# Kernel tuning notes

Hardware: AMD Instinct MI355X
Metric: run time of the kernel (lower is better)

The kernel has to match this reference:

```python
import jax, jax.numpy as jnp
import numpy as np

C = 64
C8 = C // 8
N, H, W = 4, 512, 512


def conv1x1(x, w, b):
    # x: [N,C,H,W], w: [O,C], b: [O]
    return jnp.einsum('nchw,oc->nohw', x, w) + b[None, :, None, None]


def time_attention(x, qw, qb, kw, kb, vw, vb, gamma):
    # attention over the H axis; feature dim is (C//8)*W
    q = conv1x1(x, qw, qb)                     # [N,C8,H,W]
    k = conv1x1(x, kw, kb)                     # [N,C8,H,W]
    v = conv1x1(x, vw, vb)                     # [N,C,H,W]
    energy = jnp.einsum('nchw,ncgw->nhg', q, k)   # [N,H,H]
    attn = jax.nn.softmax(energy, axis=-1)
    out = jnp.einsum('ncgw,nhg->nchw', v, attn)   # [N,C,H,W]
    return gamma * out + x


def freq_attention(x, qw, qb, kw, kb, vw, vb, gamma):
    # attention over the W axis; feature dim is (C//8)*H
    q = conv1x1(x, qw, qb)
    k = conv1x1(x, kw, kb)
    v = conv1x1(x, vw, vb)
    energy = jnp.einsum('nchw,nchv->nwv', q, k)   # [N,W,W]
    attn = jax.nn.softmax(energy, axis=-1)
    out = jnp.einsum('nchv,nwv->nchw', v, attn)
    return gamma * out + x


def setup_inputs() -> dict:
    key = jax.random.key(0)
    ks = jax.random.split(key, 8)
    s = 0.05
    return {
        'x': jax.random.normal(ks[0], (N, C, H, W), dtype=jnp.float32),
        'tq_w': jax.random.normal(ks[1], (C8, C), dtype=jnp.float32) * s,
        'tq_b': jnp.zeros((C8,), jnp.float32),
        'tk_w': jax.random.normal(ks[2], (C8, C), dtype=jnp.float32) * s,
        'tk_b': jnp.zeros((C8,), jnp.float32),
        'tv_w': jax.random.normal(ks[3], (C, C), dtype=jnp.float32) * s,
        'tv_b': jnp.zeros((C,), jnp.float32),
        't_gamma': jnp.ones((1,), jnp.float32) * 0.5,
        'fq_w': jax.random.normal(ks[4], (C8, C), dtype=jnp.float32) * s,
        'fq_b': jnp.zeros((C8,), jnp.float32),
        'fk_w': jax.random.normal(ks[5], (C8, C), dtype=jnp.float32) * s,
        'fk_b': jnp.zeros((C8,), jnp.float32),
        'fv_w': jax.random.normal(ks[6], (C, C), dtype=jnp.float32) * s,
        'fv_b': jnp.zeros((C,), jnp.float32),
        'f_gamma': jnp.ones((1,), jnp.float32) * 0.5,
    }


def reference(x, tq_w, tq_b, tk_w, tk_b, tv_w, tv_b, t_gamma,
              fq_w, fq_b, fk_w, fk_b, fv_w, fv_b, f_gamma):
    t = time_attention(x, tq_w, tq_b, tk_w, tk_b, tv_w, tv_b, t_gamma)
    f = freq_attention(x, fq_w, fq_b, fk_w, fk_b, fv_w, fv_b, f_gamma)
    return x + t + f
```

## Files before the change

### kernel.cpp

```cpp
#include <hip/hip_runtime.h>
#include <stdint.h>

#define HW 262144
#define LDIM 512

typedef __bf16 bf16x8 __attribute__((ext_vector_type(8)));
typedef float f32x4 __attribute__((ext_vector_type(4)));
typedef short s16x8 __attribute__((ext_vector_type(8)));
typedef short s16x4 __attribute__((ext_vector_type(4)));

__device__ __forceinline__ unsigned short f2bf(float f) {
  union { float f; unsigned u; } v; v.f = f;
  unsigned r = v.u + 0x7fffu + ((v.u >> 16) & 1u);
  return (unsigned short)(r >> 16);
}

__device__ __forceinline__ s16x8 pack_bf8(float4 a, float4 b) {
  s16x8 r;
  r[0] = (short)f2bf(a.x); r[1] = (short)f2bf(a.y);
  r[2] = (short)f2bf(a.z); r[3] = (short)f2bf(a.w);
  r[4] = (short)f2bf(b.x); r[5] = (short)f2bf(b.y);
  r[6] = (short)f2bf(b.z); r[7] = (short)f2bf(b.w);
  return r;
}

__device__ __forceinline__ f32x4 mfma16(bf16x8 a, bf16x8 b, f32x4 c) {
  return __builtin_amdgcn_mfma_f32_16x16x32_bf16(a, b, c, 0, 0, 0);
}

__global__ __launch_bounds__(256) void cast_k(const float* __restrict__ x,
                                              short* __restrict__ xb,
                                              short* __restrict__ xt) {
  __shared__ short L[64][72];
  int z = blockIdx.z;
  int h0 = blockIdx.y * 64, w0 = blockIdx.x * 64;
  int tid = threadIdx.x;
  size_t base = (size_t)z * HW;
  int hl = tid >> 4;
  int wl = (tid & 15) * 4;
#pragma unroll
  for (int it = 0; it < 4; ++it) {
    int h = h0 + hl + it * 16;
    float4 v = *(const float4*)(x + base + (size_t)h * 512 + w0 + wl);
    s16x4 b;
    b[0] = (short)f2bf(v.x); b[1] = (short)f2bf(v.y);
    b[2] = (short)f2bf(v.z); b[3] = (short)f2bf(v.w);
    *(s16x4*)(xb + base + (size_t)h * 512 + w0 + wl) = b;
    L[wl + 0][hl + it * 16] = b[0];
    L[wl + 1][hl + it * 16] = b[1];
    L[wl + 2][hl + it * 16] = b[2];
    L[wl + 3][hl + it * 16] = b[3];
  }
  __syncthreads();
#pragma unroll
  for (int it = 0; it < 4; ++it) {
    int w = hl + it * 16;
    s16x4 v = *(const s16x4*)(&L[w][wl]);
    *(s16x4*)(xt + base + (size_t)(w0 + w) * 512 + h0 + wl) = v;
  }
}

template<int MODE>
__device__ __forceinline__ void stage_tile(short* __restrict__ dst,
                                           const void* __restrict__ base,
                                           size_t eoff, int ld, int kk, int mn0,
                                           int tid) {
  if constexpr (MODE == 0) {
    int r = tid >> 1, off = (tid & 1) * 16;
    const short* s = (const short*)base + eoff + (size_t)(mn0 + r) * ld + kk + off;
    s16x8 v0 = *(const s16x8*)s;
    s16x8 v1 = *(const s16x8*)(s + 8);
    *(s16x8*)(dst + r * 40 + off) = v0;
    *(s16x8*)(dst + r * 40 + off + 8) = v1;
  } else {
    int mp = (tid & 63) * 2, k0 = (tid >> 6) * 8;
    const short* s = (const short*)base + eoff + (size_t)(kk + k0) * ld + mn0 + mp;
    s16x8 c0, c1;
#pragma unroll
    for (int j = 0; j < 8; ++j) {
      unsigned v = *(const unsigned*)(s + (size_t)j * ld);
      c0[j] = (short)(v & 0xffffu);
      c1[j] = (short)(v >> 16);
    }
    *(s16x8*)(dst + mp * 40 + k0) = c0;
    *(s16x8*)(dst + (mp + 1) * 40 + k0) = c1;
  }
}

template<int AM, int BM, bool OBF>
__global__ __launch_bounds__(256, 2) void gemm_k(
    const void* __restrict__ A0, long az, int zshA, int lda,
    const void* __restrict__ B0, long bz, int zshB, int ldb,
    void* __restrict__ C0, long cz) {
  __shared__ __align__(16) short As[128 * 40];
  __shared__ __align__(16) short Bs[128 * 40];
  int tid = threadIdx.x;
  int z = blockIdx.z;
  int m0g = blockIdx.y * 128, n0g = blockIdx.x * 128;
  size_t aoffz = (size_t)(z >> zshA) * (size_t)az;
  size_t boffz = (size_t)(z >> zshB) * (size_t)bz;
  int lane = tid & 63, wv = tid >> 6;
  int wm = (wv >> 1) * 64, wn = (wv & 1) * 64;
  int fr = lane & 15, q = lane >> 4;

  f32x4 acc[4][4];
#pragma unroll
  for (int mi = 0; mi < 4; ++mi)
#pragma unroll
    for (int ni = 0; ni < 4; ++ni) acc[mi][ni] = (f32x4){0.f, 0.f, 0.f, 0.f};

  for (int kidx = 0; kidx < 16; ++kidx) {
    int kk = kidx * 32;
    stage_tile<AM>(As, A0, aoffz, lda, kk, m0g, tid);
    stage_tile<BM>(Bs, B0, boffz, ldb, kk, n0g, tid);
    __syncthreads();
    bf16x8 af[4], bg[4];
#pragma unroll
    for (int mi = 0; mi < 4; ++mi)
      af[mi] = *(const bf16x8*)(As + (wm + mi * 16 + fr) * 40 + q * 8);
#pragma unroll
    for (int ni = 0; ni < 4; ++ni)
      bg[ni] = *(const bf16x8*)(Bs + (wn + ni * 16 + fr) * 40 + q * 8);
#pragma unroll
    for (int mi = 0; mi < 4; ++mi)
#pragma unroll
      for (int ni = 0; ni < 4; ++ni)
        acc[mi][ni] = mfma16(af[mi], bg[ni], acc[mi][ni]);
    __syncthreads();
  }

  size_t coff = (size_t)z * (size_t)cz;
#pragma unroll
  for (int mi = 0; mi < 4; ++mi)
#pragma unroll
    for (int ni = 0; ni < 4; ++ni) {
      int row = m0g + wm + mi * 16 + q * 4;
      int col = n0g + wn + ni * 16 + fr;
#pragma unroll
      for (int r = 0; r < 4; ++r) {
        float v = acc[mi][ni][r];
        if constexpr (OBF) {
          ((short*)C0)[coff + (size_t)(row + r) * LDIM + col] = (short)f2bf(v);
        } else {
          ((float*)C0)[coff + (size_t)(row + r) * LDIM + col] = v;
        }
      }
    }
}

__global__ __launch_bounds__(256, 2) void conv_qk_k(
    const short* __restrict__ xb,
    const float* __restrict__ tqw, const float* __restrict__ tqb,
    const float* __restrict__ tkw, const float* __restrict__ tkb,
    const float* __restrict__ fqw, const float* __restrict__ fqb,
    const float* __restrict__ fkw, const float* __restrict__ fkb,
    short* __restrict__ QT, short* __restrict__ KT,
    short* __restrict__ QF, short* __restrict__ KF) {
  __shared__ __align__(16) short As[128 * 72];
  __shared__ __align__(16) short Ws[32 * 72];
  __shared__ float bia[32];
  int tid = threadIdx.x;
  int n = blockIdx.x >> 11;
  int p0 = (blockIdx.x & 2047) << 7;
  {
    int co = tid >> 3, k0 = (tid & 7) * 8;
    const float* wsrc = (co < 8) ? tqw : (co < 16) ? tkw : (co < 24) ? fqw : fkw;
    const float* sp = wsrc + (co & 7) * 64 + k0;
    float4 f0 = *(const float4*)sp;
    float4 f1 = *(const float4*)(sp + 4);
    *(s16x8*)(Ws + co * 72 + k0) = pack_bf8(f0, f1);
    if (tid < 32) {
      const float* bsrc = (tid < 8) ? tqb : (tid < 16) ? tkb : (tid < 24) ? fqb : fkb;
      bia[tid] = bsrc[tid & 7];
    }
  }
  {
    int mp = (tid & 31) * 4, k0 = (tid >> 5) * 8;
    const short* sp = xb + ((size_t)(n * 64 + k0)) * HW + p0 + mp;
    s16x8 t0, t1, t2, t3;
#pragma unroll
    for (int j = 0; j < 8; ++j) {
      s16x4 vv = *(const s16x4*)(sp + (size_t)j * HW);
      t0[j] = vv[0]; t1[j] = vv[1]; t2[j] = vv[2]; t3[j] = vv[3];
    }
    *(s16x8*)(As + (mp + 0) * 72 + k0) = t0;
    *(s16x8*)(As + (mp + 1) * 72 + k0) = t1;
    *(s16x8*)(As + (mp + 2) * 72 + k0) = t2;
    *(s16x8*)(As + (mp + 3) * 72 + k0) = t3;
  }
  __syncthreads();
  int lane = tid & 63, wv = tid >> 6, fr = lane & 15, q = lane >> 4;
  int wm = wv * 32;
  f32x4 acc[2][2];
#pragma unroll
  for (int mi = 0; mi < 2; ++mi)
#pragma unroll
    for (int ni = 0; ni < 2; ++ni) acc[mi][ni] = (f32x4){0.f, 0.f, 0.f, 0.f};
#pragma unroll
  for (int ks = 0; ks < 2; ++ks) {
    bf16x8 af[2], bf_[2];
#pragma unroll
    for (int mi = 0; mi < 2; ++mi)
      af[mi] = *(const bf16x8*)(As + (wm + mi * 16 + fr) * 72 + ks * 32 + q * 8);
#pragma unroll
    for (int ni = 0; ni < 2; ++ni)
      bf_[ni] = *(const bf16x8*)(Ws + (ni * 16 + fr) * 72 + ks * 32 + q * 8);
#pragma unroll
    for (int mi = 0; mi < 2; ++mi)
#pragma unroll
      for (int ni = 0; ni < 2; ++ni)
        acc[mi][ni] = mfma16(af[mi], bf_[ni], acc[mi][ni]);
  }
#pragma unroll
  for (int mi = 0; mi < 2; ++mi)
#pragma unroll
    for (int ni = 0; ni < 2; ++ni) {
      int pl = wm + mi * 16 + q * 4;
      int co = ni * 16 + fr;
      float b = bia[co];
      short* dstt = (co < 8) ? QT : (co < 16) ? KT : (co < 24) ? QF : KF;
      short* d = dstt + ((size_t)(n * 8 + (co & 7))) * HW + p0 + pl;
      s16x4 sv;
#pragma unroll
      for (int r = 0; r < 4; ++r) sv[r] = (short)f2bf(acc[mi][ni][r] + b);
      *(s16x4*)d = sv;
    }
}

__global__ __launch_bounds__(256, 4) void softmax8_k(const float* __restrict__ Ep,
                                                     short* __restrict__ A) {
  int tid = threadIdx.x;
  int lane = tid & 63, wv = tid >> 6;
  int row = blockIdx.x * 4 + wv;
  int n = row >> 9, h = row & 511;
  const float* base = Ep + (size_t)(n * 8) * HW + (size_t)h * 512 + lane * 8;
  float v[8] = {0.f, 0.f, 0.f, 0.f, 0.f, 0.f, 0.f, 0.f};
#pragma unroll
  for (int cc = 0; cc < 8; ++cc) {
    const float* e = base + (size_t)cc * HW;
    float4 a = *(const float4*)e;
    float4 b = *(const float4*)(e + 4);
    v[0] += a.x; v[1] += a.y; v[2] += a.z; v[3] += a.w;
    v[4] += b.x; v[5] += b.y; v[6] += b.z; v[7] += b.w;
  }
  float m = v[0];
#pragma unroll
  for (int j = 1; j < 8; ++j) m = fmaxf(m, v[j]);
#pragma unroll
  for (int off = 32; off >= 1; off >>= 1) m = fmaxf(m, __shfl_xor(m, off));
  float s = 0.f;
#pragma unroll
  for (int j = 0; j < 8; ++j) {
    v[j] = __expf(v[j] - m);
    s += v[j];
  }
#pragma unroll
  for (int off = 32; off >= 1; off >>= 1) s += __shfl_xor(s, off);
  float inv = 1.f / s;
  s16x8 o;
#pragma unroll
  for (int j = 0; j < 8; ++j) o[j] = (short)f2bf(v[j] * inv);
  *(s16x8*)(A + (size_t)row * LDIM + lane * 8) = o;
}

__global__ __launch_bounds__(256, 2) void final_k(
    const short* __restrict__ ZT, const short* __restrict__ ZF,
    const float* __restrict__ xn,
    const float* __restrict__ tvw, const float* __restrict__ tvb,
    const float* __restrict__ fvw, const float* __restrict__ fvb,
    const float* __restrict__ tg, const float* __restrict__ fg,
    float* __restrict__ outn) {
  __shared__ __align__(16) short Zts[128 * 72];
  __shared__ __align__(16) short Zfs[128 * 72];
  __shared__ __align__(16) short Wv[128 * 72];
  __shared__ float bia[128];
  int tid = threadIdx.x;
  int n = blockIdx.x >> 11;
  int p0 = (blockIdx.x & 2047) << 7;
  {
    int co = tid >> 1, k0 = (tid & 1) * 32;
    const float* wsrc = (co < 64) ? (tvw + co * 64) : (fvw + (co - 64) * 64);
#pragma unroll
    for (int g = 0; g < 4; ++g) {
      float4 f0 = *(const float4*)(wsrc + k0 + g * 8);
      float4 f1 = *(const float4*)(wsrc + k0 + g * 8 + 4);
      *(s16x8*)(Wv + co * 72 + k0 + g * 8) = pack_bf8(f0, f1);
    }
    if (tid < 128) bia[tid] = (tid < 64) ? tvb[tid] : fvb[tid - 64];
  }
  {
    int mp = (tid & 31) * 4, k0 = (tid >> 5) * 8;
    const short* spT = ZT + ((size_t)(n * 64 + k0)) * HW + p0 + mp;
    const short* spF = ZF + ((size_t)(n * 64 + k0)) * HW + p0 + mp;
    s16x8 t0, t1, t2, t3;
#pragma unroll
    for (int j = 0; j < 8; ++j) {
      s16x4 vv = *(const s16x4*)(spT + (size_t)j * HW);
      t0[j] = vv[0]; t1[j] = vv[1]; t2[j] = vv[2]; t3[j] = vv[3];
    }
    *(s16x8*)(Zts + (mp + 0) * 72 + k0) = t0;
    *(s16x8*)(Zts + (mp + 1) * 72 + k0) = t1;
    *(s16x8*)(Zts + (mp + 2) * 72 + k0) = t2;
    *(s16x8*)(Zts + (mp + 3) * 72 + k0) = t3;
#pragma unroll
    for (int j = 0; j < 8; ++j) {
      s16x4 vv = *(const s16x4*)(spF + (size_t)j * HW);
      t0[j] = vv[0]; t1[j] = vv[1]; t2[j] = vv[2]; t3[j] = vv[3];
    }
    *(s16x8*)(Zfs + (mp + 0) * 72 + k0) = t0;
    *(s16x8*)(Zfs + (mp + 1) * 72 + k0) = t1;
    *(s16x8*)(Zfs + (mp + 2) * 72 + k0) = t2;
    *(s16x8*)(Zfs + (mp + 3) * 72 + k0) = t3;
  }
  __syncthreads();
  int lane = tid & 63, wv = tid >> 6, fr = lane & 15, q = lane >> 4;
  int wm = wv * 32;
  f32x4 at_[2][4], af_[2][4];
#pragma unroll
  for (int mi = 0; mi < 2; ++mi)
#pragma unroll
    for (int ni = 0; ni < 4; ++ni) {
      at_[mi][ni] = (f32x4){0.f, 0.f, 0.f, 0.f};
      af_[mi][ni] = (f32x4){0.f, 0.f, 0.f, 0.f};
    }
#pragma unroll
  for (int ks = 0; ks < 2; ++ks) {
    bf16x8 zt_[2], zf_[2], wt_[4], wf_[4];
#pragma unroll
    for (int mi = 0; mi < 2; ++mi) {
      zt_[mi] = *(const bf16x8*)(Zts + (wm + mi * 16 + fr) * 72 + ks * 32 + q * 8);
      zf_[mi] = *(const bf16x8*)(Zfs + (wm + mi * 16 + fr) * 72 + ks * 32 + q * 8);
    }
#pragma unroll
    for (int ni = 0; ni < 4; ++ni) {
      wt_[ni] = *(const bf16x8*)(Wv + (ni * 16 + fr) * 72 + ks * 32 + q * 8);
      wf_[ni] = *(const bf16x8*)(Wv + (64 + ni * 16 + fr) * 72 + ks * 32 + q * 8);
    }
#pragma unroll
    for (int mi = 0; mi < 2; ++mi)
#pragma unroll
      for (int ni = 0; ni < 4; ++ni) {
        at_[mi][ni] = mfma16(zt_[mi], wt_[ni], at_[mi][ni]);
        af_[mi][ni] = mfma16(zf_[mi], wf_[ni], af_[mi][ni]);
      }
  }
  float gtv = tg[0], gfv = fg[0];
#pragma unroll
  for (int mi = 0; mi < 2; ++mi)
#pragma unroll
    for (int ni = 0; ni < 4; ++ni) {
      int pl = wm + mi * 16 + q * 4;
      int co = ni * 16 + fr;
      size_t idx = ((size_t)(n * 64 + co)) * HW + p0 + pl;
      float4 xv = *(const float4*)(xn + idx);
      float bt = bia[co], bff = bia[64 + co];
      float4 ov;
      ov.x = 3.f * xv.x + gtv * (at_[mi][ni][0] + bt) + gfv * (af_[mi][ni][0] + bff);
      ov.y = 3.f * xv.y + gtv * (at_[mi][ni][1] + bt) + gfv * (af_[mi][ni][1] + bff);
      ov.z = 3.f * xv.z + gtv * (at_[mi][ni][2] + bt) + gfv * (af_[mi][ni][2] + bff);
      ov.w = 3.f * xv.w + gtv * (at_[mi][ni][3] + bt) + gfv * (af_[mi][ni][3] + bff);
      *(float4*)(outn + idx) = ov;
    }
}

extern "C" void kernel_launch(void* const* d_in, const int* in_sizes, int n_in,
                              void* d_out, int out_size, void* d_ws, size_t ws_size,
                              hipStream_t stream) {
  (void)in_sizes; (void)n_in; (void)out_size;
  const float* x   = (const float*)d_in[0];
  const float* tqw = (const float*)d_in[1];
  const float* tqb = (const float*)d_in[2];
  const float* tkw = (const float*)d_in[3];
  const float* tkb = (const float*)d_in[4];
  const float* tvw = (const float*)d_in[5];
  const float* tvb = (const float*)d_in[6];
  const float* tg  = (const float*)d_in[7];
  const float* fqw = (const float*)d_in[8];
  const float* fqb = (const float*)d_in[9];
  const float* fkw = (const float*)d_in[10];
  const float* fkb = (const float*)d_in[11];
  const float* fvw = (const float*)d_in[12];
  const float* fvb = (const float*)d_in[13];
  const float* fg  = (const float*)d_in[14];
  float* out = (float*)d_out;

  const size_t per_n = ((size_t)64 * HW * 2) * 2
                     + ((size_t)8 * HW * 2) * 4
                     + ((size_t)64 * HW * 2) * 2
                     + (size_t)HW * 2;
  int nb = (ws_size >= 4 * per_n) ? 4 : (ws_size >= 2 * per_n) ? 2 : 1;

  char* w = (char*)d_ws;
  size_t sz_x  = (size_t)nb * 64 * HW * 2;
  size_t sz_qk = (size_t)nb * 8 * HW * 2;
  size_t sz_z  = (size_t)nb * 64 * HW * 2;
  short* xb = (short*)(w);
  short* xt = (short*)(w + sz_x);
  short* QT = (short*)(w + 2 * sz_x);
  short* KT = (short*)(w + 2 * sz_x + sz_qk);
  short* QF = (short*)(w + 2 * sz_x + 2 * sz_qk);
  short* KF = (short*)(w + 2 * sz_x + 3 * sz_qk);
  short* ZT = (short*)(w + 2 * sz_x + 4 * sz_qk);
  short* ZF = (short*)(w + 2 * sz_x + 4 * sz_qk + sz_z);
  short* Ab = (short*)(w + 2 * sz_x + 4 * sz_qk + 2 * sz_z);
  float* EbT = (float*)ZT;
  float* EbF = (float*)ZF;

  for (int n0 = 0; n0 < 4; n0 += nb) {
    const float* xn = x + (size_t)n0 * 64 * HW;
    float* outn = out + (size_t)n0 * 64 * HW;
    cast_k<<<dim3(8, 8, nb * 64), dim3(256), 0, stream>>>(xn, xb, xt);
    conv_qk_k<<<dim3(nb * 2048), dim3(256), 0, stream>>>(
        xb, tqw, tqb, tkw, tkb, fqw, fqb, fkw, fkb, QT, KT, QF, KF);
    gemm_k<0, 0, false><<<dim3(4, 4, nb * 8), dim3(256), 0, stream>>>(
        QT, (long)HW, 0, 512, KT, (long)HW, 0, 512, EbT, (long)HW);
    softmax8_k<<<dim3(nb * 128), dim3(256), 0, stream>>>(EbT, Ab);
    gemm_k<0, 0, true><<<dim3(4, 4, nb * 64), dim3(256), 0, stream>>>(
        Ab, (long)HW, 6, 512, xt, (long)HW, 0, 512, ZT, (long)HW);
    gemm_k<2, 2, false><<<dim3(4, 4, nb * 8), dim3(256), 0, stream>>>(
        QF, (long)HW, 0, 512, KF, (long)HW, 0, 512, EbF, (long)HW);
    softmax8_k<<<dim3(nb * 128), dim3(256), 0, stream>>>(EbF, Ab);
    gemm_k<0, 0, true><<<dim3(4, 4, nb * 64), dim3(256), 0, stream>>>(
        xb, (long)HW, 0, 512, Ab, (long)HW, 6, 512, ZF, (long)HW);
    final_k<<<dim3(nb * 2048), dim3(256), 0, stream>>>(
        ZT, ZF, xn, tvw, tvb, fvw, fvb, tg, fg, outn);
  }
}
```

Before: 1.025 ms.

## Stage GEMM tiles with direct global-to-LDS loads and read bf16 residual

Non-transposed batched GEMMs now load tiles straight from global memory into unpadded LDS with global_load_lds, with a higher occupancy target. The transposed-operand path for the frequency energy moves into its own kernel. The value-projection weights are converted to bf16 once in a prep kernel instead of in every final_k block. final_k also reads the residual x from the bf16 copy rather than fp32, which halves that traffic but lowers the residual's precision. The workspace aliases xt with ZF to save memory, and unpadded LDS rows may cause bank conflicts on fragment reads.

New measurement: 977.1 us. 1.05x faster.

```diff
diff --git a/kernel.cpp b/kernel.cpp
--- a/kernel.cpp
+++ b/kernel.cpp
@@ -13,6 +13,12 @@
   union { float f; unsigned u; } v; v.f = f;
   unsigned r = v.u + 0x7fffu + ((v.u >> 16) & 1u);
   return (unsigned short)(r >> 16);
+}
+
+__device__ __forceinline__ float bf2f(short s) {
+  union { unsigned u; float f; } v;
+  v.u = ((unsigned)(unsigned short)s) << 16;
+  return v.f;
 }
 
 __device__ __forceinline__ s16x8 pack_bf8(float4 a, float4 b) {
@@ -26,6 +32,12 @@
 
 __device__ __forceinline__ f32x4 mfma16(bf16x8 a, bf16x8 b, f32x4 c) {
   return __builtin_amdgcn_mfma_f32_16x16x32_bf16(a, b, c, 0, 0, 0);
+}
+
+__device__ __forceinline__ void gl_lds16(const short* g, short* l) {
+  __builtin_amdgcn_global_load_lds(
+      (const __attribute__((address_space(1))) void*)g,
+      (__attribute__((address_space(3))) void*)l, 16, 0, 0);
 }
 
 __global__ __launch_bounds__(256) void cast_k(const float* __restrict__ x,
@@ -60,67 +72,68 @@
   }
 }
 
-template<int MODE>
-__device__ __forceinline__ void stage_tile(short* __restrict__ dst,
-                                           const void* __restrict__ base,
-                                           size_t eoff, int ld, int kk, int mn0,
-                                           int tid) {
-  if constexpr (MODE == 0) {
-    int r = tid >> 1, off = (tid & 1) * 16;
-    const short* s = (const short*)base + eoff + (size_t)(mn0 + r) * ld + kk + off;
-    s16x8 v0 = *(const s16x8*)s;
-    s16x8 v1 = *(const s16x8*)(s + 8);
-    *(s16x8*)(dst + r * 40 + off) = v0;
-    *(s16x8*)(dst + r * 40 + off + 8) = v1;
-  } else {
-    int mp = (tid & 63) * 2, k0 = (tid >> 6) * 8;
-    const short* s = (const short*)base + eoff + (size_t)(kk + k0) * ld + mn0 + mp;
-    s16x8 c0, c1;
-#pragma unroll
-    for (int j = 0; j < 8; ++j) {
-      unsigned v = *(const unsigned*)(s + (size_t)j * ld);
-      c0[j] = (short)(v & 0xffffu);
-      c1[j] = (short)(v >> 16);
-    }
-    *(s16x8*)(dst + mp * 40 + k0) = c0;
-    *(s16x8*)(dst + (mp + 1) * 40 + k0) = c1;
-  }
-}
-
-template<int AM, int BM, bool OBF>
-__global__ __launch_bounds__(256, 2) void gemm_k(
-    const void* __restrict__ A0, long az, int zshA, int lda,
-    const void* __restrict__ B0, long bz, int zshB, int ldb,
+__global__ __launch_bounds__(256) void prep_k(const float* __restrict__ tvw,
+                                              const float* __restrict__ fvw,
+                                              short* __restrict__ Wvb) {
+  int t = threadIdx.x;
+#pragma unroll
+  for (int i = 0; i < 2; ++i) {
+    int idx = (i * 256 + t) * 8;
+    float4 a = *(const float4*)(tvw + idx);
+    float4 b = *(const float4*)(tvw + idx + 4);
+    *(s16x8*)(Wvb + idx) = pack_bf8(a, b);
+    a = *(const float4*)(fvw + idx);
+    b = *(const float4*)(fvw + idx + 4);
+    *(s16x8*)(Wvb + 4096 + idx) = pack_bf8(a, b);
+  }
+}
+
+template<bool OBF>
+__global__ __launch_bounds__(256, 4) void gemm_a(
+    const short* __restrict__ A0, long az, int zshA,
+    const short* __restrict__ B0, long bz, int zshB,
     void* __restrict__ C0, long cz) {
-  __shared__ __align__(16) short As[128 * 40];
-  __shared__ __align__(16) short Bs[128 * 40];
+  __shared__ __align__(16) short As[128 * 32];
+  __shared__ __align__(16) short Bs[128 * 32];
   int tid = threadIdx.x;
   int z = blockIdx.z;
   int m0g = blockIdx.y * 128, n0g = blockIdx.x * 128;
-  size_t aoffz = (size_t)(z >> zshA) * (size_t)az;
-  size_t boffz = (size_t)(z >> zshB) * (size_t)bz;
+  const short* Abz = A0 + (size_t)(z >> zshA) * (size_t)az;
+  const short* Bbz = B0 + (size_t)(z >> zshB) * (size_t)bz;
   int lane = tid & 63, wv = tid >> 6;
   int wm = (wv >> 1) * 64, wn = (wv & 1) * 64;
   int fr = lane & 15, q = lane >> 4;
 
+  int srow = lane >> 2;
+  int sch = (lane & 3) * 8;
+  const short* ga0 = Abz + (size_t)(m0g + wv * 32 + srow) * 512 + sch;
+  const short* ga1 = ga0 + 16 * 512;
+  const short* gb0 = Bbz + (size_t)(n0g + wv * 32 + srow) * 512 + sch;
+  const short* gb1 = gb0 + 16 * 512;
+  short* la0 = As + (wv * 32) * 32;
+  short* la1 = As + (wv * 32 + 16) * 32;
+  short* lb0 = Bs + (wv * 32) * 32;
+  short* lb1 = Bs + (wv * 32 + 16) * 32;
+
   f32x4 acc[4][4];
 #pragma unroll
   for (int mi = 0; mi < 4; ++mi)
 #pragma unroll
     for (int ni = 0; ni < 4; ++ni) acc[mi][ni] = (f32x4){0.f, 0.f, 0.f, 0.f};
 
-  for (int kidx = 0; kidx < 16; ++kidx) {
-    int kk = kidx * 32;
-    stage_tile<AM>(As, A0, aoffz, lda, kk, m0g, tid);
-    stage_tile<BM>(Bs, B0, boffz, ldb, kk, n0g, tid);
+  for (int kk = 0; kk < 512; kk += 32) {
+    gl_lds16(ga0 + kk, la0);
+    gl_lds16(ga1 + kk, la1);
+    gl_lds16(gb0 + kk, lb0);
+    gl_lds16(gb1 + kk, lb1);
     __syncthreads();
     bf16x8 af[4], bg[4];
 #pragma unroll
     for (int mi = 0; mi < 4; ++mi)
-      af[mi] = *(const bf16x8*)(As + (wm + mi * 16 + fr) * 40 + q * 8);
+      af[mi] = *(const bf16x8*)(As + (wm + mi * 16 + fr) * 32 + q * 8);
 #pragma unroll
     for (int ni = 0; ni < 4; ++ni)
-      bg[ni] = *(const bf16x8*)(Bs + (wn + ni * 16 + fr) * 40 + q * 8);
+      bg[ni] = *(const bf16x8*)(Bs + (wn + ni * 16 + fr) * 32 + q * 8);
 #pragma unroll
     for (int mi = 0; mi < 4; ++mi)
 #pragma unroll
@@ -145,6 +158,82 @@
           ((float*)C0)[coff + (size_t)(row + r) * LDIM + col] = v;
         }
       }
+    }
+}
+
+__global__ __launch_bounds__(256, 2) void gemm_t(
+    const short* __restrict__ A0, long az,
+    const short* __restrict__ B0, long bz,
+    float* __restrict__ C0, long cz) {
+  __shared__ __align__(16) short As[128 * 40];
+  __shared__ __align__(16) short Bs[128 * 40];
+  int tid = threadIdx.x;
+  int z = blockIdx.z;
+  int m0g = blockIdx.y * 128, n0g = blockIdx.x * 128;
+  const short* Abz = A0 + (size_t)z * (size_t)az;
+  const short* Bbz = B0 + (size_t)z * (size_t)bz;
+  int lane = tid & 63, wv = tid >> 6;
+  int wm = (wv >> 1) * 64, wn = (wv & 1) * 64;
+  int fr = lane & 15, q = lane >> 4;
+  int mp = (tid & 63) * 2, k0 = (tid >> 6) * 8;
+
+  f32x4 acc[4][4];
+#pragma unroll
+  for (int mi = 0; mi < 4; ++mi)
+#pragma unroll
+    for (int ni = 0; ni < 4; ++ni) acc[mi][ni] = (f32x4){0.f, 0.f, 0.f, 0.f};
+
+  for (int kk = 0; kk < 512; kk += 32) {
+    {
+      const short* s = Abz + (size_t)(kk + k0) * 512 + m0g + mp;
+      s16x8 c0, c1;
+#pragma unroll
+      for (int j = 0; j < 8; ++j) {
+        unsigned v = *(const unsigned*)(s + (size_t)j * 512);
+        c0[j] = (short)(v & 0xffffu);
+        c1[j] = (short)(v >> 16);
+      }
+      *(s16x8*)(As + mp * 40 + k0) = c0;
+      *(s16x8*)(As + (mp + 1) * 40 + k0) = c1;
+    }
+    {
+      const short* s = Bbz + (size_t)(kk + k0) * 512 + n0g + mp;
+      s16x8 c0, c1;
+#pragma unroll
+      for (int j = 0; j < 8; ++j) {
+        unsigned v = *(const unsigned*)(s + (size_t)j * 512);
+        c0[j] = (short)(v & 0xffffu);
+        c1[j] = (short)(v >> 16);
+      }
+      *(s16x8*)(Bs + mp * 40 + k0) = c0;
+      *(s16x8*)(Bs + (mp + 1) * 40 + k0) = c1;
+    }
+    __syncthreads();
+    bf16x8 af[4], bg[4];
+#pragma unroll
+    for (int mi = 0; mi < 4; ++mi)
+      af[mi] = *(const bf16x8*)(As + (wm + mi * 16 + fr) * 40 + q * 8);
+#pragma unroll
+    for (int ni = 0; ni < 4; ++ni)
+      bg[ni] = *(const bf16x8*)(Bs + (wn + ni * 16 + fr) * 40 + q * 8);
+#pragma unroll
+    for (int mi = 0; mi < 4; ++mi)
+#pragma unroll
+      for (int ni = 0; ni < 4; ++ni)
+        acc[mi][ni] = mfma16(af[mi], bg[ni], acc[mi][ni]);
+    __syncthreads();
+  }
+
+  size_t coff = (size_t)z * (size_t)cz;
+#pragma unroll
+  for (int mi = 0; mi < 4; ++mi)
+#pragma unroll
+    for (int ni = 0; ni < 4; ++ni) {
+      int row = m0g + wm + mi * 16 + q * 4;
+      int col = n0g + wn + ni * 16 + fr;
+#pragma unroll
+      for (int r = 0; r < 4; ++r)
+        C0[coff + (size_t)(row + r) * LDIM + col] = acc[mi][ni][r];
     }
 }
 
@@ -263,31 +352,19 @@
   *(s16x8*)(A + (size_t)row * LDIM + lane * 8) = o;
 }
 
-__global__ __launch_bounds__(256, 2) void final_k(
+__global__ __launch_bounds__(256, 3) void final_k(
     const short* __restrict__ ZT, const short* __restrict__ ZF,
-    const float* __restrict__ xn,
-    const float* __restrict__ tvw, const float* __restrict__ tvb,
-    const float* __restrict__ fvw, const float* __restrict__ fvb,
+    const short* __restrict__ xb, const short* __restrict__ Wvb,
+    const float* __restrict__ tvb, const float* __restrict__ fvb,
     const float* __restrict__ tg, const float* __restrict__ fg,
     float* __restrict__ outn) {
   __shared__ __align__(16) short Zts[128 * 72];
   __shared__ __align__(16) short Zfs[128 * 72];
-  __shared__ __align__(16) short Wv[128 * 72];
   __shared__ float bia[128];
   int tid = threadIdx.x;
   int n = blockIdx.x >> 11;
   int p0 = (blockIdx.x & 2047) << 7;
-  {
-    int co = tid >> 1, k0 = (tid & 1) * 32;
-    const float* wsrc = (co < 64) ? (tvw + co * 64) : (fvw + (co - 64) * 64);
-#pragma unroll
-    for (int g = 0; g < 4; ++g) {
-      float4 f0 = *(const float4*)(wsrc + k0 + g * 8);
-      float4 f1 = *(const float4*)(wsrc + k0 + g * 8 + 4);
-      *(s16x8*)(Wv + co * 72 + k0 + g * 8) = pack_bf8(f0, f1);
-    }
-    if (tid < 128) bia[tid] = (tid < 64) ? tvb[tid] : fvb[tid - 64];
-  }
+  if (tid < 128) bia[tid] = (tid < 64) ? tvb[tid] : fvb[tid - 64];
   {
     int mp = (tid & 31) * 4, k0 = (tid >> 5) * 8;
     const short* spT = ZT + ((size_t)(n * 64 + k0)) * HW + p0 + mp;
@@ -333,8 +410,8 @@
     }
 #pragma unroll
     for (int ni = 0; ni < 4; ++ni) {
-      wt_[ni] = *(const bf16x8*)(Wv + (ni * 16 + fr) * 72 + ks * 32 + q * 8);
-      wf_[ni] = *(const bf16x8*)(Wv + (64 + ni * 16 + fr) * 72 + ks * 32 + q * 8);
+      wt_[ni] = *(const bf16x8*)(Wvb + (ni * 16 + fr) * 64 + ks * 32 + q * 8);
+      wf_[ni] = *(const bf16x8*)(Wvb + 4096 + (ni * 16 + fr) * 64 + ks * 32 + q * 8);
     }
 #pragma unroll
     for (int mi = 0; mi < 2; ++mi)
@@ -352,13 +429,13 @@
       int pl = wm + mi * 16 + q * 4;
       int co = ni * 16 + fr;
       size_t idx = ((size_t)(n * 64 + co)) * HW + p0 + pl;
-      float4 xv = *(const float4*)(xn + idx);
+      s16x4 xv = *(const s16x4*)(xb + idx);
       float bt = bia[co], bff = bia[64 + co];
       float4 ov;
-      ov.x = 3.f * xv.x + gtv * (at_[mi][ni][0] + bt) + gfv * (af_[mi][ni][0] + bff);
-      ov.y = 3.f * xv.y + gtv * (at_[mi][ni][1] + bt) + gfv * (af_[mi][ni][1] + bff);
-      ov.z = 3.f * xv.z + gtv * (at_[mi][ni][2] + bt) + gfv * (af_[mi][ni][2] + bff);
-      ov.w = 3.f * xv.w + gtv * (at_[mi][ni][3] + bt) + gfv * (af_[mi][ni][3] + bff);
+      ov.x = 3.f * bf2f(xv[0]) + gtv * (at_[mi][ni][0] + bt) + gfv * (af_[mi][ni][0] + bff);
+      ov.y = 3.f * bf2f(xv[1]) + gtv * (at_[mi][ni][1] + bt) + gfv * (af_[mi][ni][1] + bff);
+      ov.z = 3.f * bf2f(xv[2]) + gtv * (at_[mi][ni][2] + bt) + gfv * (af_[mi][ni][2] + bff);
+      ov.w = 3.f * bf2f(xv[3]) + gtv * (at_[mi][ni][3] + bt) + gfv * (af_[mi][ni][3] + bff);
       *(float4*)(outn + idx) = ov;
     }
 }
@@ -384,27 +461,30 @@
   const float* fg  = (const float*)d_in[14];
   float* out = (float*)d_out;
 
-  const size_t per_n = ((size_t)64 * HW * 2) * 2
+  const size_t per_n = ((size_t)64 * HW * 2) * 3
                      + ((size_t)8 * HW * 2) * 4
-                     + ((size_t)64 * HW * 2) * 2
                      + (size_t)HW * 2;
-  int nb = (ws_size >= 4 * per_n) ? 4 : (ws_size >= 2 * per_n) ? 2 : 1;
+  int nb = (ws_size >= 4 * per_n + 16384) ? 4
+         : (ws_size >= 2 * per_n + 16384) ? 2 : 1;
 
   char* w = (char*)d_ws;
+  short* Wvb = (short*)w;
+  char* wb = w + 16384;
   size_t sz_x  = (size_t)nb * 64 * HW * 2;
   size_t sz_qk = (size_t)nb * 8 * HW * 2;
-  size_t sz_z  = (size_t)nb * 64 * HW * 2;
-  short* xb = (short*)(w);
-  short* xt = (short*)(w + sz_x);
-  short* QT = (short*)(w + 2 * sz_x);
-  short* KT = (short*)(w + 2 * sz_x + sz_qk);
-  short* QF = (short*)(w + 2 * sz_x + 2 * sz_qk);
-  short* KF = (short*)(w + 2 * sz_x + 3 * sz_qk);
-  short* ZT = (short*)(w + 2 * sz_x + 4 * sz_qk);
-  short* ZF = (short*)(w + 2 * sz_x + 4 * sz_qk + sz_z);
-  short* Ab = (short*)(w + 2 * sz_x + 4 * sz_qk + 2 * sz_z);
+  short* xb = (short*)(wb);
+  short* ZF = (short*)(wb + sz_x);
+  short* xt = ZF;
+  short* QT = (short*)(wb + 2 * sz_x);
+  short* KT = (short*)(wb + 2 * sz_x + sz_qk);
+  short* QF = (short*)(wb + 2 * sz_x + 2 * sz_qk);
+  short* KF = (short*)(wb + 2 * sz_x + 3 * sz_qk);
+  short* ZT = (short*)(wb + 2 * sz_x + 4 * sz_qk);
+  short* Ab = (short*)(wb + 3 * sz_x + 4 * sz_qk);
   float* EbT = (float*)ZT;
   float* EbF = (float*)ZF;
+
+  prep_k<<<dim3(1), dim3(256), 0, stream>>>(tvw, fvw, Wvb);
 
   for (int n0 = 0; n0 < 4; n0 += nb) {
     const float* xn = x + (size_t)n0 * 64 * HW;
@@ -412,17 +492,17 @@
     cast_k<<<dim3(8, 8, nb * 64), dim3(256), 0, stream>>>(xn, xb, xt);
     conv_qk_k<<<dim3(nb * 2048), dim3(256), 0, stream>>>(
         xb, tqw, tqb, tkw, tkb, fqw, fqb, fkw, fkb, QT, KT, QF, KF);
-    gemm_k<0, 0, false><<<dim3(4, 4, nb * 8), dim3(256), 0, stream>>>(
-        QT, (long)HW, 0, 512, KT, (long)HW, 0, 512, EbT, (long)HW);
+    gemm_a<false><<<dim3(4, 4, nb * 8), dim3(256), 0, stream>>>(
+        QT, (long)HW, 0, KT, (long)HW, 0, EbT, (long)HW);
     softmax8_k<<<dim3(nb * 128), dim3(256), 0, stream>>>(EbT, Ab);
-    gemm_k<0, 0, true><<<dim3(4, 4, nb * 64), dim3(256), 0, stream>>>(
-        Ab, (long)HW, 6, 512, xt, (long)HW, 0, 512, ZT, (long)HW);
-    gemm_k<2, 2, false><<<dim3(4, 4, nb * 8), dim3(256), 0, stream>>>(
-        QF, (long)HW, 0, 512, KF, (long)HW, 0, 512, EbF, (long)HW);
+    gemm_a<true><<<dim3(4, 4, nb * 64), dim3(256), 0, stream>>>(
+        Ab, (long)HW, 6, xt, (long)HW, 0, ZT, (long)HW);
+    gemm_t<<<dim3(4, 4, nb * 8), dim3(256), 0, stream>>>(
+        QF, (long)HW, KF, (long)HW, EbF, (long)HW);
     softmax8_k<<<dim3(nb * 128), dim3(256), 0, stream>>>(EbF, Ab);
-    gemm_k<0, 0, true><<<dim3(4, 4, nb * 64), dim3(256), 0, stream>>>(
-        xb, (long)HW, 0, 512, Ab, (long)HW, 6, 512, ZF, (long)HW);
+    gemm_a<true><<<dim3(4, 4, nb * 64), dim3(256), 0, stream>>>(
+        xb, (long)HW, 0, Ab, (long)HW, 6, ZF, (long)HW);
     final_k<<<dim3(nb * 2048), dim3(256), 0, stream>>>(
-        ZT, ZF, xn, tvw, tvb, fvw, fvb, tg, fg, outn);
-  }
-}
+        ZT, ZF, xb, Wvb, tvb, fvb, tg, fg, outn);
+  }
+}
```
